# Kernel optimization log

Measured on AMD Instinct MI355X. Metric: run time of the kernel, lower is better.

Reference implementation:

```python
import jax, jax.numpy as jnp
import numpy as np

N = 20000      # nodes
E = 320000     # edges (before self-loops)
IN = 128       # in_features
H = 8          # heads
C = 120        # out channels per head
SLOPE = 0.2    # LeakyReLU negative slope (PyG default)


def setup_inputs() -> dict:
    key = jax.random.key(0)
    k = jax.random.split(key, 8)
    x = jax.random.normal(k[0], (N, IN), jnp.float32)
    edge_index = jax.random.randint(k[1], (2, E), 0, N)  # [2,E], row0=src, row1=dst
    W = jax.random.normal(k[2], (IN, H * C), jnp.float32) / np.sqrt(IN)
    att_src = jax.random.normal(k[3], (H, C), jnp.float32) * 0.1
    att_dst = jax.random.normal(k[4], (H, C), jnp.float32) * 0.1
    bias = jnp.zeros((H * C,), jnp.float32)
    fc_w = jax.random.normal(k[5], (H * C, 2), jnp.float32) / np.sqrt(H * C)
    fc_b = jnp.zeros((2,), jnp.float32)
    return dict(x=x, edge_index=edge_index, W=W, att_src=att_src,
                att_dst=att_dst, bias=bias, fc_w=fc_w, fc_b=fc_b)


def reference(x, edge_index, W, att_src, att_dst, bias, fc_w, fc_b):
    n = x.shape[0]
    # add self loops (GATConv default add_self_loops=True)
    loops = jnp.arange(n, dtype=edge_index.dtype)
    ei = jnp.concatenate([edge_index, jnp.stack([loops, loops])], axis=1)
    src, dst = ei[0], ei[1]
    # per-head linear projection: [n, H, C]
    xp = (x @ W).reshape(n, H, C)
    # per-node attention logits
    a_s = jnp.einsum('nhc,hc->nh', xp, att_src)  # [n,H]
    a_d = jnp.einsum('nhc,hc->nh', xp, att_dst)  # [n,H]
    # edge-wise logits + LeakyReLU: [Etot,H]
    e = jax.nn.leaky_relu(a_s[src] + a_d[dst], SLOPE)
    # segment softmax over incoming edges of each destination node
    emax = jax.lax.stop_gradient(jax.ops.segment_max(e, dst, num_segments=n))
    ee = jnp.exp(e - emax[dst])
    denom = jax.ops.segment_sum(ee, dst, num_segments=n)
    alpha = ee / denom[dst]                      # [Etot,H]
    # scatter-aggregate weighted messages: [n,H,C]
    out = jax.ops.segment_sum(alpha[:, :, None] * xp[src], dst, num_segments=n)
    out = out.reshape(n, H * C) + bias           # concat heads + bias
    return out @ fc_w + fc_b                     # final Linear -> [n,2]
```

## Files before the change

kernel.cpp:

```cpp
#include <hip/hip_runtime.h>

#define NN    20000
#define EDGES 320000
#define HH    8
#define CC    120
#define HC    960
#define SLOPE 0.2f
#define BUCKET 64


__global__ __launch_bounds__(256) void prep_kernel(const float* __restrict__ W,
                                                   const float* __restrict__ att_src,
                                                   const float* __restrict__ att_dst,
                                                   const float* __restrict__ bias,
                                                   const float* __restrict__ fc_w,
                                                   const float* __restrict__ fc_b,
                                                   float* __restrict__ U,
                                                   float* __restrict__ cbias,
                                                   unsigned* __restrict__ cnt) {
  int t = threadIdx.x, b = blockIdx.x;
  int gid = b * 256 + t;
  if (gid < NN) cnt[gid] = 0u;

  int l = t & 63;
  if (b < 256) {
    int p = b * 4 + (t >> 6);
    int k = p >> 3, h = p & 7;
    const float* wrow = W + (size_t)k * HC + h * CC;
    const float* asv  = att_src + h * CC;
    const float* adv  = att_dst + h * CC;
    const float2* fv  = (const float2*)fc_w + h * CC;
    bool tail = (l < CC - 64);
    float w0 = wrow[l],            w1 = tail ? wrow[64 + l] : 0.f;
    float s0 = asv[l],             s1 = tail ? asv[64 + l] : 0.f;
    float d0 = adv[l],             d1 = tail ? adv[64 + l] : 0.f;
    float2 f0 = fv[l];
    float2 f1 = tail ? fv[64 + l] : make_float2(0.f, 0.f);
    float a_s = w0 * s0 + w1 * s1;
    float a_d = w0 * d0 + w1 * d1;
    float z0  = w0 * f0.x + w1 * f1.x;
    float z1  = w0 * f0.y + w1 * f1.y;
#pragma unroll
    for (int m = 1; m < 64; m <<= 1) {
      a_s += __shfl_xor(a_s, m);
      a_d += __shfl_xor(a_d, m);
      z0  += __shfl_xor(z0, m);
      z1  += __shfl_xor(z1, m);
    }
    if (l == 0) {
      float* u = U + k * 32 + 4 * h;
      u[0] = a_s; u[1] = z0; u[2] = z1; u[3] = a_d;
    }
  } else if (b == 256 && t < 128) {
    int j = t >> 6;
    float acc = 0.f;
    for (int m = l; m < HC; m += 64) acc = fmaf(bias[m], fc_w[m * 2 + j], acc);
#pragma unroll
    for (int m = 1; m < 64; m <<= 1) acc += __shfl_xor(acc, m);
    if (l == 0) cbias[j] = acc + fc_b[j];
  }
}

#define XSTR 132
__global__ __launch_bounds__(128) void projscatter_kernel(const float* __restrict__ x,
                                                          const float* __restrict__ U,
                                                          const int* __restrict__ ei,
                                                          unsigned* __restrict__ cnt,
                                                          unsigned* __restrict__ list,
                                                          float* __restrict__ P) {
  __shared__ float xs[32 * XSTR];
  __shared__ float Us[128 * 32];
  int t = threadIdx.x;
  int b = blockIdx.x;
  int n0 = b * 32;

  const float4* xg = (const float4*)(x + (size_t)n0 * 128);
  const float4* U4 = (const float4*)U;
  float4 xv[8], uv[8];
#pragma unroll
  for (int j = 0; j < 8; ++j) xv[j] = xg[t + j * 128];
#pragma unroll
  for (int j = 0; j < 8; ++j) uv[j] = U4[t + j * 128];

  int g = b * 512 + t;
  int s0 = ei[g],           s1 = ei[g + 128];
  int s2 = ei[g + 256],     s3 = ei[g + 384];
  int d0 = ei[EDGES + g],       d1 = ei[EDGES + g + 128];
  int d2 = ei[EDGES + g + 256], d3 = ei[EDGES + g + 384];
  unsigned sl0 = atomicAdd(&cnt[d0], 1u);
  unsigned sl1 = atomicAdd(&cnt[d1], 1u);
  unsigned sl2 = atomicAdd(&cnt[d2], 1u);
  unsigned sl3 = atomicAdd(&cnt[d3], 1u);

#pragma unroll
  for (int j = 0; j < 8; ++j) {
    int i = t + j * 128;
    *(float4*)(xs + (i >> 5) * XSTR + (i & 31) * 4) = xv[j];
    ((float4*)Us)[i] = uv[j];
  }
  __syncthreads();

  int rq = t >> 3, cq = t & 7;
  float a00 = 0.f, a01 = 0.f, a02 = 0.f, a03 = 0.f;
  float a10 = 0.f, a11 = 0.f, a12 = 0.f, a13 = 0.f;
  const float* xr0 = xs + rq * XSTR;
  const float* xr1 = xs + (rq + 16) * XSTR;
#pragma unroll 4
  for (int k4 = 0; k4 < 32; ++k4) {
    float4 xa = *(const float4*)(xr0 + k4 * 4);
    float4 xb = *(const float4*)(xr1 + k4 * 4);
    float4 u0 = *(const float4*)(Us + (k4 * 4 + 0) * 32 + 4 * cq);
    float4 u1 = *(const float4*)(Us + (k4 * 4 + 1) * 32 + 4 * cq);
    float4 u2 = *(const float4*)(Us + (k4 * 4 + 2) * 32 + 4 * cq);
    float4 u3 = *(const float4*)(Us + (k4 * 4 + 3) * 32 + 4 * cq);
    a00 = fmaf(xa.x, u0.x, a00); a01 = fmaf(xa.x, u0.y, a01);
    a02 = fmaf(xa.x, u0.z, a02); a03 = fmaf(xa.x, u0.w, a03);
    a10 = fmaf(xb.x, u0.x, a10); a11 = fmaf(xb.x, u0.y, a11);
    a12 = fmaf(xb.x, u0.z, a12); a13 = fmaf(xb.x, u0.w, a13);
    a00 = fmaf(xa.y, u1.x, a00); a01 = fmaf(xa.y, u1.y, a01);
    a02 = fmaf(xa.y, u1.z, a02); a03 = fmaf(xa.y, u1.w, a03);
    a10 = fmaf(xb.y, u1.x, a10); a11 = fmaf(xb.y, u1.y, a11);
    a12 = fmaf(xb.y, u1.z, a12); a13 = fmaf(xb.y, u1.w, a13);
    a00 = fmaf(xa.z, u2.x, a00); a01 = fmaf(xa.z, u2.y, a01);
    a02 = fmaf(xa.z, u2.z, a02); a03 = fmaf(xa.z, u2.w, a03);
    a10 = fmaf(xb.z, u2.x, a10); a11 = fmaf(xb.z, u2.y, a11);
    a12 = fmaf(xb.z, u2.z, a12); a13 = fmaf(xb.z, u2.w, a13);
    a00 = fmaf(xa.w, u3.x, a00); a01 = fmaf(xa.w, u3.y, a01);
    a02 = fmaf(xa.w, u3.z, a02); a03 = fmaf(xa.w, u3.w, a03);
    a10 = fmaf(xb.w, u3.x, a10); a11 = fmaf(xb.w, u3.y, a11);
    a12 = fmaf(xb.w, u3.z, a12); a13 = fmaf(xb.w, u3.w, a13);
  }
  *(float4*)(P + (size_t)(n0 + rq) * 32 + 4 * cq) =
      make_float4(a00, a01, a02, a03);
  *(float4*)(P + (size_t)(n0 + rq + 16) * 32 + 4 * cq) =
      make_float4(a10, a11, a12, a13);

  list[(size_t)d0 * BUCKET + sl0] = (unsigned)s0;
  list[(size_t)d1 * BUCKET + sl1] = (unsigned)s1;
  list[(size_t)d2 * BUCKET + sl2] = (unsigned)s2;
  list[(size_t)d3 * BUCKET + sl3] = (unsigned)s3;
}

__global__ __launch_bounds__(256) void gather_kernel(const unsigned* __restrict__ cnt,
                                                     const unsigned* __restrict__ list,
                                                     const float* __restrict__ P,
                                                     const float* __restrict__ cbias,
                                                     float* __restrict__ out) {
  int t = threadIdx.x;
  int wave = t >> 6;
  int lane = t & 63;
  int h = lane & 7;
  int o = lane >> 3;
  int dst = blockIdx.x * 4 + wave;

  const float* pd = P + (size_t)dst * 32;
  float4 pd4 = *(const float4*)(pd + 4 * h);
  float ad = pd4.w;
  unsigned deg = cnt[dst];
  unsigned rv = list[(size_t)dst * BUCKET + lane];

  float accd = 0.f, acc0 = 0.f, acc1 = 0.f;
  if (o == 0) {
    float v = pd4.x + ad;
    v = (v > 0.f) ? v : SLOPE * v;
    float ex = __expf(v);
    accd = ex;
    acc0 = ex * pd4.y;
    acc1 = ex * pd4.z;
  }

  unsigned e0 = o, e1 = o + 8, e2 = o + 16, e3 = o + 24;
  unsigned s0 = __shfl(rv, (int)e0);
  unsigned s1 = __shfl(rv, (int)e1);
  unsigned s2 = __shfl(rv, (int)e2);
  unsigned s3 = __shfl(rv, (int)e3);
  bool m0 = e0 < deg, m1 = e1 < deg, m2 = e2 < deg, m3 = e3 < deg;
  unsigned a0 = m0 ? s0 : (unsigned)dst;
  unsigned a1 = m1 ? s1 : (unsigned)dst;
  unsigned a2 = m2 ? s2 : (unsigned)dst;
  unsigned a3 = m3 ? s3 : (unsigned)dst;
  float4 q0 = *(const float4*)(P + (size_t)a0 * 32 + 4 * h);
  float4 q1 = *(const float4*)(P + (size_t)a1 * 32 + 4 * h);
  float4 q2 = *(const float4*)(P + (size_t)a2 * 32 + 4 * h);
  float4 q3 = *(const float4*)(P + (size_t)a3 * 32 + 4 * h);
  if (m0) {
    float v = q0.x + ad; v = (v > 0.f) ? v : SLOPE * v;
    float ex = __expf(v);
    accd += ex; acc0 = fmaf(ex, q0.y, acc0); acc1 = fmaf(ex, q0.z, acc1);
  }
  if (m1) {
    float v = q1.x + ad; v = (v > 0.f) ? v : SLOPE * v;
    float ex = __expf(v);
    accd += ex; acc0 = fmaf(ex, q1.y, acc0); acc1 = fmaf(ex, q1.z, acc1);
  }
  if (m2) {
    float v = q2.x + ad; v = (v > 0.f) ? v : SLOPE * v;
    float ex = __expf(v);
    accd += ex; acc0 = fmaf(ex, q2.y, acc0); acc1 = fmaf(ex, q2.z, acc1);
  }
  if (m3) {
    float v = q3.x + ad; v = (v > 0.f) ? v : SLOPE * v;
    float ex = __expf(v);
    accd += ex; acc0 = fmaf(ex, q3.y, acc0); acc1 = fmaf(ex, q3.z, acc1);
  }
  if (deg > 32u) {
    unsigned iters = (deg - 32u + 7u) >> 3;
    unsigned e = 32u + (unsigned)o;
    for (unsigned i = 0; i < iters; ++i, e += 8u) {
      unsigned src = __shfl(rv, (int)e);
      if (e < deg) {
        float4 q = *(const float4*)(P + (size_t)src * 32 + 4 * h);
        float v = q.x + ad; v = (v > 0.f) ? v : SLOPE * v;
        float ex = __expf(v);
        accd += ex; acc0 = fmaf(ex, q.y, acc0); acc1 = fmaf(ex, q.z, acc1);
      }
    }
  }
  float accd_tot = accd + __shfl_xor(accd, 8);
  accd_tot += __shfl_xor(accd_tot, 16);
  accd_tot += __shfl_xor(accd_tot, 32);
  float rcp = 1.0f / accd_tot;
  float r0 = acc0 * rcp;
  float r1 = acc1 * rcp;
#pragma unroll
  for (int m = 1; m < 64; m <<= 1) {
    r0 += __shfl_xor(r0, m);
    r1 += __shfl_xor(r1, m);
  }
  if (lane == 0) {
    ((float2*)out)[dst] = make_float2(cbias[0] + r0, cbias[1] + r1);
  }
}

extern "C" void kernel_launch(void* const* d_in, const int* in_sizes, int n_in,
                              void* d_out, int out_size, void* d_ws, size_t ws_size,
                              hipStream_t stream) {
  const float* x       = (const float*)d_in[0];
  const int*   ei      = (const int*)d_in[1];
  const float* W       = (const float*)d_in[2];
  const float* att_src = (const float*)d_in[3];
  const float* att_dst = (const float*)d_in[4];
  const float* bias    = (const float*)d_in[5];
  const float* fc_w    = (const float*)d_in[6];
  const float* fc_b    = (const float*)d_in[7];
  float* out = (float*)d_out;

  float*    U     = (float*)d_ws;
  float*    cbias = U + 4096;
  float*    P     = U + 8192;
  unsigned* cnt   = (unsigned*)(P + (size_t)NN * 32);
  unsigned* list  = cnt + NN;

  prep_kernel<<<257, 256, 0, stream>>>(W, att_src, att_dst, bias, fc_w, fc_b, U, cbias, cnt);
  projscatter_kernel<<<NN / 32, 128, 0, stream>>>(x, U, ei, cnt, list, P);
  gather_kernel<<<NN / 4, 256, 0, stream>>>(cnt, list, P, cbias, out);
}
```

Measured before the change: 41.00 us.

## Replace global atomic bucketing with per-chunk LDS histograms and prefix scan

```diff
diff --git a/kernel.cpp b/kernel.cpp
--- a/kernel.cpp
+++ b/kernel.cpp
@@ -7,6 +7,9 @@
 #define HC    960
 #define SLOPE 0.2f
 #define BUCKET 64
+#define NB    128
+#define CH    (EDGES / NB)
+#define NPAIR (NN / 2)
 
 
 __global__ __launch_bounds__(256) void prep_kernel(const float* __restrict__ W,
@@ -15,13 +18,12 @@
                                                    const float* __restrict__ bias,
                                                    const float* __restrict__ fc_w,
                                                    const float* __restrict__ fc_b,
+                                                   const int* __restrict__ ei,
                                                    float* __restrict__ U,
                                                    float* __restrict__ cbias,
-                                                   unsigned* __restrict__ cnt) {
+                                                   unsigned* __restrict__ hist) {
+  __shared__ unsigned hsh[NPAIR];
   int t = threadIdx.x, b = blockIdx.x;
-  int gid = b * 256 + t;
-  if (gid < NN) cnt[gid] = 0u;
-
   int l = t & 63;
   if (b < 256) {
     int p = b * 4 + (t >> 6);
@@ -51,97 +53,128 @@
       float* u = U + k * 32 + 4 * h;
       u[0] = a_s; u[1] = z0; u[2] = z1; u[3] = a_d;
     }
-  } else if (b == 256 && t < 128) {
-    int j = t >> 6;
-    float acc = 0.f;
-    for (int m = l; m < HC; m += 64) acc = fmaf(bias[m], fc_w[m * 2 + j], acc);
-#pragma unroll
-    for (int m = 1; m < 64; m <<= 1) acc += __shfl_xor(acc, m);
-    if (l == 0) cbias[j] = acc + fc_b[j];
-  }
+  } else if (b == 256) {
+    if (t < 128) {
+      int j = t >> 6;
+      float acc = 0.f;
+      for (int m = l; m < HC; m += 64) acc = fmaf(bias[m], fc_w[m * 2 + j], acc);
+#pragma unroll
+      for (int m = 1; m < 64; m <<= 1) acc += __shfl_xor(acc, m);
+      if (l == 0) cbias[j] = acc + fc_b[j];
+    }
+  } else {
+    int c = b - 257;
+    for (int i = t; i < NPAIR; i += 256) hsh[i] = 0u;
+    __syncthreads();
+    const int* dsts = ei + EDGES + c * CH;
+    for (int i = t; i < CH; i += 256) {
+      int d = dsts[i];
+      atomicAdd(&hsh[d >> 1], (d & 1) ? (1u << 16) : 1u);
+    }
+    __syncthreads();
+    unsigned* hrow = hist + (size_t)c * NPAIR;
+    for (int i = t; i < NPAIR; i += 256) hrow[i] = hsh[i];
+  }
+}
+
+__global__ __launch_bounds__(256) void scan_kernel(const unsigned* __restrict__ hist,
+                                                   unsigned* __restrict__ base,
+                                                   unsigned* __restrict__ deg) {
+  int j = blockIdx.x * 256 + threadIdx.x;
+  if (j >= NPAIR) return;
+  unsigned sA = 0, sB = 0;
+#pragma unroll 8
+  for (int c = 0; c < NB; ++c) {
+    unsigned v = hist[(size_t)c * NPAIR + j];
+    base[(size_t)c * NPAIR + j] = sA | (sB << 16);
+    sA += v & 0xFFFFu;
+    sB += v >> 16;
+  }
+  deg[2 * j]     = sA;
+  deg[2 * j + 1] = sB;
 }
 
 #define XSTR 132
-__global__ __launch_bounds__(128) void projscatter_kernel(const float* __restrict__ x,
-                                                          const float* __restrict__ U,
-                                                          const int* __restrict__ ei,
-                                                          unsigned* __restrict__ cnt,
-                                                          unsigned* __restrict__ list,
-                                                          float* __restrict__ P) {
-  __shared__ float xs[32 * XSTR];
-  __shared__ float Us[128 * 32];
+__global__ __launch_bounds__(128) void projplace_kernel(const float* __restrict__ x,
+                                                        const float* __restrict__ U,
+                                                        const int* __restrict__ ei,
+                                                        const unsigned* __restrict__ base,
+                                                        unsigned* __restrict__ list,
+                                                        float* __restrict__ P) {
+  __shared__ unsigned smem[NPAIR];
   int t = threadIdx.x;
   int b = blockIdx.x;
-  int n0 = b * 32;
-
-  const float4* xg = (const float4*)(x + (size_t)n0 * 128);
-  const float4* U4 = (const float4*)U;
-  float4 xv[8], uv[8];
-#pragma unroll
-  for (int j = 0; j < 8; ++j) xv[j] = xg[t + j * 128];
-#pragma unroll
-  for (int j = 0; j < 8; ++j) uv[j] = U4[t + j * 128];
-
-  int g = b * 512 + t;
-  int s0 = ei[g],           s1 = ei[g + 128];
-  int s2 = ei[g + 256],     s3 = ei[g + 384];
-  int d0 = ei[EDGES + g],       d1 = ei[EDGES + g + 128];
-  int d2 = ei[EDGES + g + 256], d3 = ei[EDGES + g + 384];
-  unsigned sl0 = atomicAdd(&cnt[d0], 1u);
-  unsigned sl1 = atomicAdd(&cnt[d1], 1u);
-  unsigned sl2 = atomicAdd(&cnt[d2], 1u);
-  unsigned sl3 = atomicAdd(&cnt[d3], 1u);
-
-#pragma unroll
-  for (int j = 0; j < 8; ++j) {
-    int i = t + j * 128;
-    *(float4*)(xs + (i >> 5) * XSTR + (i & 31) * 4) = xv[j];
-    ((float4*)Us)[i] = uv[j];
-  }
-  __syncthreads();
-
-  int rq = t >> 3, cq = t & 7;
-  float a00 = 0.f, a01 = 0.f, a02 = 0.f, a03 = 0.f;
-  float a10 = 0.f, a11 = 0.f, a12 = 0.f, a13 = 0.f;
-  const float* xr0 = xs + rq * XSTR;
-  const float* xr1 = xs + (rq + 16) * XSTR;
+
+  if (b < 625) {
+    float* xs = (float*)smem;
+    float* Us = (float*)smem + 32 * XSTR;
+    int n0 = b * 32;
+    const float4* xg = (const float4*)(x + (size_t)n0 * 128);
+    const float4* U4 = (const float4*)U;
+    float4 xv[8], uv[8];
+#pragma unroll
+    for (int j = 0; j < 8; ++j) xv[j] = xg[t + j * 128];
+#pragma unroll
+    for (int j = 0; j < 8; ++j) uv[j] = U4[t + j * 128];
+#pragma unroll
+    for (int j = 0; j < 8; ++j) {
+      int i = t + j * 128;
+      *(float4*)(xs + (i >> 5) * XSTR + (i & 31) * 4) = xv[j];
+      ((float4*)Us)[i] = uv[j];
+    }
+    __syncthreads();
+
+    int rq = t >> 3, cq = t & 7;
+    float a00 = 0.f, a01 = 0.f, a02 = 0.f, a03 = 0.f;
+    float a10 = 0.f, a11 = 0.f, a12 = 0.f, a13 = 0.f;
+    const float* xr0 = xs + rq * XSTR;
+    const float* xr1 = xs + (rq + 16) * XSTR;
 #pragma unroll 4
-  for (int k4 = 0; k4 < 32; ++k4) {
-    float4 xa = *(const float4*)(xr0 + k4 * 4);
-    float4 xb = *(const float4*)(xr1 + k4 * 4);
-    float4 u0 = *(const float4*)(Us + (k4 * 4 + 0) * 32 + 4 * cq);
-    float4 u1 = *(const float4*)(Us + (k4 * 4 + 1) * 32 + 4 * cq);
-    float4 u2 = *(const float4*)(Us + (k4 * 4 + 2) * 32 + 4 * cq);
-    float4 u3 = *(const float4*)(Us + (k4 * 4 + 3) * 32 + 4 * cq);
-    a00 = fmaf(xa.x, u0.x, a00); a01 = fmaf(xa.x, u0.y, a01);
-    a02 = fmaf(xa.x, u0.z, a02); a03 = fmaf(xa.x, u0.w, a03);
-    a10 = fmaf(xb.x, u0.x, a10); a11 = fmaf(xb.x, u0.y, a11);
-    a12 = fmaf(xb.x, u0.z, a12); a13 = fmaf(xb.x, u0.w, a13);
-    a00 = fmaf(xa.y, u1.x, a00); a01 = fmaf(xa.y, u1.y, a01);
-    a02 = fmaf(xa.y, u1.z, a02); a03 = fmaf(xa.y, u1.w, a03);
-    a10 = fmaf(xb.y, u1.x, a10); a11 = fmaf(xb.y, u1.y, a11);
-    a12 = fmaf(xb.y, u1.z, a12); a13 = fmaf(xb.y, u1.w, a13);
-    a00 = fmaf(xa.z, u2.x, a00); a01 = fmaf(xa.z, u2.y, a01);
-    a02 = fmaf(xa.z, u2.z, a02); a03 = fmaf(xa.z, u2.w, a03);
-    a10 = fmaf(xb.z, u2.x, a10); a11 = fmaf(xb.z, u2.y, a11);
-    a12 = fmaf(xb.z, u2.z, a12); a13 = fmaf(xb.z, u2.w, a13);
-    a00 = fmaf(xa.w, u3.x, a00); a01 = fmaf(xa.w, u3.y, a01);
-    a02 = fmaf(xa.w, u3.z, a02); a03 = fmaf(xa.w, u3.w, a03);
-    a10 = fmaf(xb.w, u3.x, a10); a11 = fmaf(xb.w, u3.y, a11);
-    a12 = fmaf(xb.w, u3.z, a12); a13 = fmaf(xb.w, u3.w, a13);
-  }
-  *(float4*)(P + (size_t)(n0 + rq) * 32 + 4 * cq) =
-      make_float4(a00, a01, a02, a03);
-  *(float4*)(P + (size_t)(n0 + rq + 16) * 32 + 4 * cq) =
-      make_float4(a10, a11, a12, a13);
-
-  list[(size_t)d0 * BUCKET + sl0] = (unsigned)s0;
-  list[(size_t)d1 * BUCKET + sl1] = (unsigned)s1;
-  list[(size_t)d2 * BUCKET + sl2] = (unsigned)s2;
-  list[(size_t)d3 * BUCKET + sl3] = (unsigned)s3;
-}
-
-__global__ __launch_bounds__(256) void gather_kernel(const unsigned* __restrict__ cnt,
+    for (int k4 = 0; k4 < 32; ++k4) {
+      float4 xa = *(const float4*)(xr0 + k4 * 4);
+      float4 xb = *(const float4*)(xr1 + k4 * 4);
+      float4 u0 = *(const float4*)(Us + (k4 * 4 + 0) * 32 + 4 * cq);
+      float4 u1 = *(const float4*)(Us + (k4 * 4 + 1) * 32 + 4 * cq);
+      float4 u2 = *(const float4*)(Us + (k4 * 4 + 2) * 32 + 4 * cq);
+      float4 u3 = *(const float4*)(Us + (k4 * 4 + 3) * 32 + 4 * cq);
+      a00 = fmaf(xa.x, u0.x, a00); a01 = fmaf(xa.x, u0.y, a01);
+      a02 = fmaf(xa.x, u0.z, a02); a03 = fmaf(xa.x, u0.w, a03);
+      a10 = fmaf(xb.x, u0.x, a10); a11 = fmaf(xb.x, u0.y, a11);
+      a12 = fmaf(xb.x, u0.z, a12); a13 = fmaf(xb.x, u0.w, a13);
+      a00 = fmaf(xa.y, u1.x, a00); a01 = fmaf(xa.y, u1.y, a01);
+      a02 = fmaf(xa.y, u1.z, a02); a03 = fmaf(xa.y, u1.w, a03);
+      a10 = fmaf(xb.y, u1.x, a10); a11 = fmaf(xb.y, u1.y, a11);
+      a12 = fmaf(xb.y, u1.z, a12); a13 = fmaf(xb.y, u1.w, a13);
+      a00 = fmaf(xa.z, u2.x, a00); a01 = fmaf(xa.z, u2.y, a01);
+      a02 = fmaf(xa.z, u2.z, a02); a03 = fmaf(xa.z, u2.w, a03);
+      a10 = fmaf(xb.z, u2.x, a10); a11 = fmaf(xb.z, u2.y, a11);
+      a12 = fmaf(xb.z, u2.z, a12); a13 = fmaf(xb.z, u2.w, a13);
+      a00 = fmaf(xa.w, u3.x, a00); a01 = fmaf(xa.w, u3.y, a01);
+      a02 = fmaf(xa.w, u3.z, a02); a03 = fmaf(xa.w, u3.w, a03);
+      a10 = fmaf(xb.w, u3.x, a10); a11 = fmaf(xb.w, u3.y, a11);
+      a12 = fmaf(xb.w, u3.z, a12); a13 = fmaf(xb.w, u3.w, a13);
+    }
+    *(float4*)(P + (size_t)(n0 + rq) * 32 + 4 * cq) =
+        make_float4(a00, a01, a02, a03);
+    *(float4*)(P + (size_t)(n0 + rq + 16) * 32 + 4 * cq) =
+        make_float4(a10, a11, a12, a13);
+  } else {
+    int c = b - 625;
+    for (int i = t; i < NPAIR; i += 128)
+      smem[i] = base[(size_t)c * NPAIR + i];
+    __syncthreads();
+    const int* srcs = ei + c * CH;
+    const int* dsts = ei + EDGES + c * CH;
+    for (int i = t; i < CH; i += 128) {
+      int s = srcs[i], d = dsts[i];
+      unsigned old = atomicAdd(&smem[d >> 1], (d & 1) ? (1u << 16) : 1u);
+      unsigned slot = (d & 1) ? (old >> 16) : (old & 0xFFFFu);
+      list[(size_t)d * BUCKET + slot] = (unsigned)s;
+    }
+  }
+}
+
+__global__ __launch_bounds__(256) void gather_kernel(const unsigned* __restrict__ deg_,
                                                      const unsigned* __restrict__ list,
                                                      const float* __restrict__ P,
                                                      const float* __restrict__ cbias,
@@ -156,7 +189,7 @@
   const float* pd = P + (size_t)dst * 32;
   float4 pd4 = *(const float4*)(pd + 4 * h);
   float ad = pd4.w;
-  unsigned deg = cnt[dst];
+  unsigned deg = deg_[dst];
   unsigned rv = list[(size_t)dst * BUCKET + lane];
 
   float accd = 0.f, acc0 = 0.f, acc1 = 0.f;
@@ -248,10 +281,14 @@
   float*    U     = (float*)d_ws;
   float*    cbias = U + 4096;
   float*    P     = U + 8192;
-  unsigned* cnt   = (unsigned*)(P + (size_t)NN * 32);
-  unsigned* list  = cnt + NN;
-
-  prep_kernel<<<257, 256, 0, stream>>>(W, att_src, att_dst, bias, fc_w, fc_b, U, cbias, cnt);
-  projscatter_kernel<<<NN / 32, 128, 0, stream>>>(x, U, ei, cnt, list, P);
-  gather_kernel<<<NN / 4, 256, 0, stream>>>(cnt, list, P, cbias, out);
-}
+  unsigned* deg   = (unsigned*)(P + (size_t)NN * 32);
+  unsigned* list  = deg + NN;
+  unsigned* hist  = list + (size_t)NN * BUCKET;
+  unsigned* base  = hist + (size_t)NB * NPAIR;
+
+  prep_kernel<<<385, 256, 0, stream>>>(W, att_src, att_dst, bias, fc_w, fc_b,
+                                       ei, U, cbias, hist);
+  scan_kernel<<<40, 256, 0, stream>>>(hist, base, deg);
+  projplace_kernel<<<753, 128, 0, stream>>>(x, U, ei, base, list, P);
+  gather_kernel<<<NN / 4, 256, 0, stream>>>(deg, list, P, cbias, out);
+}
```

Result: slower. 45.37 us (+10.7%).
